# Optimization experiments

Measured on AMD Instinct MI355X. Metric: run time of the kernel, lower is better.

The kernel has to match this reference:

```python
import jax, jax.numpy as jnp
import numpy as np

HEAD_SIZE = 64

def setup_inputs() -> dict:
    key = jax.random.key(0)
    k1, k2, k3, k4 = jax.random.split(key, 4)
    B, T, C = 4, 4096, 768
    s = 1.0 / np.sqrt(C)
    return {
        "x": jax.random.normal(k1, (B, T, C), dtype=jnp.float32),
        "Wq": jax.random.normal(k2, (C, HEAD_SIZE), dtype=jnp.float32) * s,
        "Wk": jax.random.normal(k3, (C, HEAD_SIZE), dtype=jnp.float32) * s,
        "Wv": jax.random.normal(k4, (C, HEAD_SIZE), dtype=jnp.float32) * s,
    }

def reference(x, Wq, Wk, Wv):
    # x: [B,T,C]; Wq/Wk/Wv: [C,H]
    T = x.shape[1]
    q = jnp.einsum('btc,ch->bth', x, Wq)
    k = jnp.einsum('btc,ch->bth', x, Wk)
    v = jnp.einsum('btc,ch->bth', x, Wv)
    scale = HEAD_SIZE ** (-0.5)
    wei = jnp.einsum('bth,bsh->bts', q, k) * scale  # [B,T,T]
    causal = jnp.tril(jnp.ones((T, T), dtype=bool))
    wei = jnp.where(causal, wei, -jnp.inf)
    wei = jax.nn.softmax(wei, axis=-1)
    # dropout p=0.0 -> identity
    out = jnp.einsum('bts,bsh->bth', wei, v)  # [B,T,H]
    return out
```

## Files before the change

### kernel.cpp

```cpp
#include <hip/hip_runtime.h>
#include <hip/hip_bf16.h>
#include <stdint.h>

typedef unsigned short u16;
typedef __attribute__((ext_vector_type(8))) __bf16 bf16x8;
typedef __attribute__((ext_vector_type(4))) float f32x4;

#define LOG2E 1.44269504088896340736f

__device__ inline u16 f2bf(float f){
  uint32_t u = __float_as_uint(f);
  u += 0x7FFFu + ((u >> 16) & 1u);
  return (u16)(u >> 16);
}
__device__ inline float bf2f(u16 v){
  return __uint_as_float(((uint32_t)v) << 16);
}

typedef const __attribute__((address_space(1))) void* gas_t;
typedef __attribute__((address_space(3))) void* las_t;
__device__ inline void gl_lds16(const void* g, void* l){
  __builtin_amdgcn_global_load_lds((gas_t)g, (las_t)l, 16, 0, 0);
}

__global__ __launch_bounds__(256) void wt_kernel(const float* __restrict__ Wq,
                                                 const float* __restrict__ Wk,
                                                 const float* __restrict__ Wv,
                                                 u16* __restrict__ wtf){
  int idx = blockIdx.x * 256 + threadIdx.x;
  if (idx >= 192 * 768) return;
  int n = idx / 768, c = idx - n * 768;
  int h = n & 63;
  const float* W = (n < 64) ? Wq : ((n < 128) ? Wk : Wv);
  float v = W[c * 64 + h];
  if (n < 64) v *= 0.125f * LOG2E;
  int f = n >> 4, n16 = n & 15;
  int kstep = c >> 5, quad = (c >> 3) & 3, j = c & 7;
  wtf[(size_t)((f * 24 + kstep) * 64 + quad * 16 + n16) * 8 + j] = f2bf(v);
}

__global__ __launch_bounds__(256) void proj_kernel(const float* __restrict__ x,
                                                   const u16* __restrict__ wtf,
                                                   u16* __restrict__ qs,
                                                   u16* __restrict__ ksf,
                                                   u16* __restrict__ vtf){
  __shared__ u16 At[24 * 64 * 8];
  const int tid = threadIdx.x;
  const int w = tid >> 6, lane = tid & 63;
  const int n16 = lane & 15, quad = lane >> 4;
  const int rt = blockIdx.x * 16;

  const float* xb = x + (size_t)rt * 768;
  float4 t[12];
#pragma unroll
  for (int i = 0; i < 12; ++i)
    t[i] = *(const float4*)(xb + (size_t)(i * 256 + tid) * 4);
#pragma unroll
  for (int i = 0; i < 12; ++i){
    int l = i * 256 + tid;
    int row = l / 192, c4 = l - row * 192;
    int ksn = c4 >> 3, qd = (c4 >> 1) & 3, j0 = (c4 & 1) * 4;
    int idx = ((ksn * 64 + qd * 16 + row) * 8 + j0) ^ ((ksn & 7) << 3);
    union { ushort4 s; u16 e[4]; } pk;
    pk.e[0] = f2bf(t[i].x); pk.e[1] = f2bf(t[i].y);
    pk.e[2] = f2bf(t[i].z); pk.e[3] = f2bf(t[i].w);
    *(ushort4*)&At[idx] = pk.s;
  }
  __syncthreads();

  const f32x4 fz = {0.f, 0.f, 0.f, 0.f};
  f32x4 acc[3];
#pragma unroll
  for (int j = 0; j < 3; ++j) acc[j] = fz;

#pragma unroll
  for (int kst = 0; kst < 24; ++kst){
    const int sw = (kst & 7) << 3;
    bf16x8 a = *(const bf16x8*)&At[((kst * 64 + lane) * 8) ^ sw];
#pragma unroll
    for (int j = 0; j < 3; ++j){
      bf16x8 bfr = *(const bf16x8*)(wtf + (size_t)(((3 * w + j) * 24 + kst) * 64 + lane) * 8);
      acc[j] = __builtin_amdgcn_mfma_f32_16x16x32_bf16(a, bfr, acc[j], 0, 0, 0);
    }
  }
  __syncthreads();

#pragma unroll
  for (int j = 0; j < 3; ++j){
    const int F = 3 * w + j;
    const int s = F >> 2, c0 = (F & 3) * 16;
#pragma unroll
    for (int r = 0; r < 4; ++r){
      u16 val = f2bf(acc[j][r]);
      int row = quad * 4 + r;
      if (s < 2) At[s * 1152 + row * 72 + c0 + n16] = val;
      else       At[2304 + (c0 + n16) * 24 + row]   = val;
    }
  }
  __syncthreads();

  const int bb = rt >> 12, t0 = rt & 4095;
  const int kt = t0 >> 6;
  const int fk = (t0 >> 4) & 3;
  const int half0 = (t0 >> 5) & 1;
  const int qhalf = (t0 >> 4) & 1;
  if (tid < 128){
    int row = tid >> 3, hc = tid & 7;
    uint4 qv = *(const uint4*)&At[row * 72 + hc * 8];
    *(uint4*)(qs + (size_t)(rt + row) * 64 + hc * 8) = qv;
  } else {
    int tt = tid - 128;
    int half = tt >> 6, l2 = tt & 63;
    int nn = l2 & 15, qq = l2 >> 4;
    uint4 kv = *(const uint4*)&At[1152 + nn * 72 + half * 32 + qq * 8];
    size_t off = ((((size_t)(bb * 64 + kt) * 4 + fk) * 2 + half) * 64 + l2) * 8;
    *(uint4*)(ksf + off) = kv;
  }
  if (tid < 128){
    int f = tid >> 5, idx5 = tid & 31;
    int qsel = idx5 >> 4, nn = idx5 & 15;
    int h = f * 16 + nn;
    uint4 vv = *(const uint4*)&At[2304 + h * 24 + qsel * 8];
    int lane2 = (2 * qhalf + qsel) * 16 + nn;
    size_t off = ((((size_t)(bb * 64 + kt) * 4 + f) * 2 + half0) * 64 + lane2) * 8;
    *(uint4*)(vtf + off) = vv;
  }
}

__global__ __launch_bounds__(256) void flash_part(const u16* __restrict__ qs,
                                                  const u16* __restrict__ ksf,
                                                  const u16* __restrict__ vtf,
                                                  u16* __restrict__ Opart,
                                                  float* __restrict__ ml){
  const int b  = blockIdx.x >> 9;
  const int qt = (blockIdx.x >> 4) & 31;
  const int ck = blockIdx.x & 15;
  const int kt0 = ck * 4;
  const int ktmax = 2 * qt + 1;
  if (kt0 > ktmax) return;
  const int nt = min(ktmax, kt0 + 3) - kt0 + 1;

  __shared__ u16 Kb[2][4096];
  __shared__ u16 Vb[2][4096];
  __shared__ u16 Ps[128 * 72];
  const int tid = threadIdx.x;
  const int w = tid >> 6, lane = tid & 63;
  const int n16 = lane & 15, quad = lane >> 4;

  const u16* qb  = qs  + (size_t)b * 262144;
  const u16* kpg = ksf + (size_t)b * 262144 + (size_t)kt0 * 4096;
  const u16* vpg = vtf + (size_t)b * 262144 + (size_t)kt0 * 4096;

  bf16x8 qA[2][2];
#pragma unroll
  for (int m = 0; m < 2; ++m){
    const size_t qrow = (size_t)(qt * 128 + w * 32 + m * 16 + n16) * 64;
    qA[m][0] = *(const bf16x8*)(qb + qrow + quad * 8);
    qA[m][1] = *(const bf16x8*)(qb + qrow + 32 + quad * 8);
  }

  const f32x4 fz = {0.f, 0.f, 0.f, 0.f};
  f32x4 O[2][4];
  float rs[2][4];
#pragma unroll
  for (int m = 0; m < 2; ++m)
#pragma unroll
    for (int f = 0; f < 4; ++f){ O[m][f] = fz; rs[m][f] = 0.f; }

#define STAGE(bf, ti)                                                        \
  {                                                                          \
    const u16* kg = kpg + (size_t)(ti) * 4096 + (w * 2) * 512 + lane * 8;    \
    const u16* vg = vpg + (size_t)(ti) * 4096 + (w * 2) * 512 + lane * 8;    \
    gl_lds16(kg,       &Kb[bf][(w * 2 + 0) * 512]);                          \
    gl_lds16(kg + 512, &Kb[bf][(w * 2 + 1) * 512]);                          \
    gl_lds16(vg,       &Vb[bf][(w * 2 + 0) * 512]);                          \
    gl_lds16(vg + 512, &Vb[bf][(w * 2 + 1) * 512]);                          \
  }

  STAGE(0, 0);
  __syncthreads();
  int c = 0;

  for (int it = 0; it < nt; ++it){
    const int kt = kt0 + it;
    if (it + 1 < nt) STAGE(c ^ 1, it + 1);

    f32x4 S[2][4];
#pragma unroll
    for (int f = 0; f < 4; ++f){
      bf16x8 k0 = *(const bf16x8*)&Kb[c][(f * 2 + 0) * 512 + lane * 8];
      bf16x8 k1 = *(const bf16x8*)&Kb[c][(f * 2 + 1) * 512 + lane * 8];
#pragma unroll
      for (int m = 0; m < 2; ++m){
        f32x4 s = fz;
        s = __builtin_amdgcn_mfma_f32_16x16x32_bf16(qA[m][0], k0, s, 0, 0, 0);
        s = __builtin_amdgcn_mfma_f32_16x16x32_bf16(qA[m][1], k1, s, 0, 0, 0);
        S[m][f] = s;
      }
    }

    if (kt >= 2 * qt){
#pragma unroll
      for (int m = 0; m < 2; ++m)
#pragma unroll
        for (int f = 0; f < 4; ++f)
#pragma unroll
          for (int r = 0; r < 4; ++r){
            int col = kt * 64 + f * 16 + n16;
            int row = qt * 128 + w * 32 + m * 16 + quad * 4 + r;
            if (col > row) S[m][f][r] = -1e30f;
          }
    }

#pragma unroll
    for (int m = 0; m < 2; ++m)
#pragma unroll
      for (int f = 0; f < 4; ++f)
#pragma unroll
        for (int r = 0; r < 4; ++r){
          float p = __builtin_amdgcn_exp2f(S[m][f][r]);
          S[m][f][r] = p;
          rs[m][r] += p;
        }

#pragma unroll
    for (int m = 0; m < 2; ++m)
#pragma unroll
      for (int f = 0; f < 4; ++f){
        u16* p = &Ps[(w * 32 + m * 16 + quad * 4) * 72 + f * 16 + n16];
        p[0]   = f2bf(S[m][f][0]);
        p[72]  = f2bf(S[m][f][1]);
        p[144] = f2bf(S[m][f][2]);
        p[216] = f2bf(S[m][f][3]);
      }
    bf16x8 pA[2][2];
#pragma unroll
    for (int m = 0; m < 2; ++m){
      pA[m][0] = *(const bf16x8*)&Ps[(w * 32 + m * 16 + n16) * 72 + quad * 8];
      pA[m][1] = *(const bf16x8*)&Ps[(w * 32 + m * 16 + n16) * 72 + 32 + quad * 8];
    }

#pragma unroll
    for (int f = 0; f < 4; ++f){
      bf16x8 v0 = *(const bf16x8*)&Vb[c][(f * 2 + 0) * 512 + lane * 8];
      bf16x8 v1 = *(const bf16x8*)&Vb[c][(f * 2 + 1) * 512 + lane * 8];
#pragma unroll
      for (int m = 0; m < 2; ++m){
        O[m][f] = __builtin_amdgcn_mfma_f32_16x16x32_bf16(pA[m][0], v0, O[m][f], 0, 0, 0);
        O[m][f] = __builtin_amdgcn_mfma_f32_16x16x32_bf16(pA[m][1], v1, O[m][f], 0, 0, 0);
      }
    }

    __syncthreads();
    c ^= 1;
  }
#undef STAGE

#pragma unroll
  for (int m = 0; m < 2; ++m)
#pragma unroll
    for (int r = 0; r < 4; ++r){
#pragma unroll
      for (int off = 1; off < 16; off <<= 1)
        rs[m][r] += __shfl_xor(rs[m][r], off, 16);
    }

  const size_t oidx = (size_t)blockIdx.x * 8192;
#pragma unroll
  for (int m = 0; m < 2; ++m)
#pragma unroll
    for (int f = 0; f < 4; ++f)
#pragma unroll
      for (int r = 0; r < 4; ++r){
        int row_local = w * 32 + m * 16 + quad * 4 + r;
        Opart[oidx + (size_t)row_local * 64 + f * 16 + n16] = f2bf(O[m][f][r]);
      }
  if (n16 == 0){
    float* lp = ml + (size_t)blockIdx.x * 128;
#pragma unroll
    for (int m = 0; m < 2; ++m)
#pragma unroll
      for (int r = 0; r < 4; ++r)
        lp[w * 32 + m * 16 + quad * 4 + r] = rs[m][r];
  }
}

__global__ __launch_bounds__(256) void combine_kernel(const u16* __restrict__ Opart,
                                                      const float* __restrict__ ml,
                                                      float* __restrict__ out){
  const int gid = blockIdx.x * 256 + threadIdx.x;
  const int bq = gid >> 11;
  const int rem = (gid & 2047) * 4;
  const int row = rem >> 6;
  const int qt = bq & 31;
  const int nc = (2 * qt + 5) >> 2;

  float L = 0.f;
  float a0 = 0.f, a1 = 0.f, a2 = 0.f, a3 = 0.f;
  for (int c = 0; c < nc; ++c){
    L += ml[((size_t)bq * 16 + c) * 128 + row];
    const u16* p = Opart + ((size_t)bq * 16 + c) * 8192 + rem;
    uint2 d = *(const uint2*)p;
    a0 += bf2f((u16)(d.x & 0xffffu));
    a1 += bf2f((u16)(d.x >> 16));
    a2 += bf2f((u16)(d.y & 0xffffu));
    a3 += bf2f((u16)(d.y >> 16));
  }
  const float invL = 1.0f / L;
  float4 v = {a0 * invL, a1 * invL, a2 * invL, a3 * invL};
  *(float4*)(out + (size_t)gid * 4) = v;
}

extern "C" void kernel_launch(void* const* d_in, const int* in_sizes, int n_in,
                              void* d_out, int out_size, void* d_ws, size_t ws_size,
                              hipStream_t stream){
  const float* x  = (const float*)d_in[0];
  const float* Wq = (const float*)d_in[1];
  const float* Wk = (const float*)d_in[2];
  const float* Wv = (const float*)d_in[3];
  float* out = (float*)d_out;

  u16* qs  = (u16*)d_ws;
  u16* ksf = qs  + (size_t)16384 * 64;
  u16* vtf = ksf + (size_t)16384 * 64;
  u16* wtf = vtf + (size_t)16384 * 64;
  u16* Opart = wtf + (size_t)192 * 768;
  float* ml = (float*)(Opart + (size_t)2048 * 8192);

  wt_kernel<<<576, 256, 0, stream>>>(Wq, Wk, Wv, wtf);
  proj_kernel<<<1024, 256, 0, stream>>>(x, wtf, qs, ksf, vtf);
  flash_part<<<2048, 256, 0, stream>>>(qs, ksf, vtf, Opart, ml);
  combine_kernel<<<1024, 256, 0, stream>>>(Opart, ml, out);
}
```

Before: 139.9 us.

## Compact causal work grid and single-buffer K/V staging in flash kernel

Replaces the 2048-block grid, where many blocks exit early on the causal mask, with a dense 1088-block grid. The new grid maps block ids to (qt, chunk) pairs through an integer square-root decode: full 4-tile chunks come first and 2-tile diagonal chunks after. The combine kernel is updated to the new partial-result indexing. K/V staging drops from double buffering to a single buffer with sync before and after each load, which halves that LDS use and may raise occupancy, but the next tile's load no longer overlaps compute.

```diff
diff --git a/kernel.cpp b/kernel.cpp
--- a/kernel.cpp
+++ b/kernel.cpp
@@ -1,6 +1,7 @@
 #include <hip/hip_runtime.h>
 #include <hip/hip_bf16.h>
 #include <stdint.h>
+#include <math.h>
 
 typedef unsigned short u16;
 typedef __attribute__((ext_vector_type(8))) __bf16 bf16x8;
@@ -132,16 +133,28 @@
                                                   const u16* __restrict__ vtf,
                                                   u16* __restrict__ Opart,
                                                   float* __restrict__ ml){
-  const int b  = blockIdx.x >> 9;
-  const int qt = (blockIdx.x >> 4) & 31;
-  const int ck = blockIdx.x & 15;
+  const int gid = blockIdx.x;
+  int b, qt, ck, nt;
+  if (gid < 1024){
+    b = gid >> 8;
+    int r = gid & 255;
+    int m = (int)sqrtf((float)r);
+    if (m * m > r) --m;
+    if ((m + 1) * (m + 1) <= r) ++m;
+    int d = r - m * m;
+    if (d < m){ qt = 2 * m;     ck = d;     }
+    else      { qt = 2 * m + 1; ck = d - m; }
+    nt = 4;
+  } else {
+    int t = gid - 1024;
+    b = t >> 4;
+    int m = t & 15;
+    qt = 2 * m; ck = m; nt = 2;
+  }
   const int kt0 = ck * 4;
-  const int ktmax = 2 * qt + 1;
-  if (kt0 > ktmax) return;
-  const int nt = min(ktmax, kt0 + 3) - kt0 + 1;
-
-  __shared__ u16 Kb[2][4096];
-  __shared__ u16 Vb[2][4096];
+
+  __shared__ u16 Kb[4096];
+  __shared__ u16 Vb[4096];
   __shared__ u16 Ps[128 * 72];
   const int tid = threadIdx.x;
   const int w = tid >> 6, lane = tid & 63;
@@ -167,29 +180,27 @@
 #pragma unroll
     for (int f = 0; f < 4; ++f){ O[m][f] = fz; rs[m][f] = 0.f; }
 
-#define STAGE(bf, ti)                                                        \
+#define STAGE(ti)                                                            \
   {                                                                          \
     const u16* kg = kpg + (size_t)(ti) * 4096 + (w * 2) * 512 + lane * 8;    \
     const u16* vg = vpg + (size_t)(ti) * 4096 + (w * 2) * 512 + lane * 8;    \
-    gl_lds16(kg,       &Kb[bf][(w * 2 + 0) * 512]);                          \
-    gl_lds16(kg + 512, &Kb[bf][(w * 2 + 1) * 512]);                          \
-    gl_lds16(vg,       &Vb[bf][(w * 2 + 0) * 512]);                          \
-    gl_lds16(vg + 512, &Vb[bf][(w * 2 + 1) * 512]);                          \
-  }
-
-  STAGE(0, 0);
-  __syncthreads();
-  int c = 0;
+    gl_lds16(kg,       &Kb[(w * 2 + 0) * 512]);                              \
+    gl_lds16(kg + 512, &Kb[(w * 2 + 1) * 512]);                              \
+    gl_lds16(vg,       &Vb[(w * 2 + 0) * 512]);                              \
+    gl_lds16(vg + 512, &Vb[(w * 2 + 1) * 512]);                              \
+  }
 
   for (int it = 0; it < nt; ++it){
     const int kt = kt0 + it;
-    if (it + 1 < nt) STAGE(c ^ 1, it + 1);
+    if (it) __syncthreads();
+    STAGE(it);
+    __syncthreads();
 
     f32x4 S[2][4];
 #pragma unroll
     for (int f = 0; f < 4; ++f){
-      bf16x8 k0 = *(const bf16x8*)&Kb[c][(f * 2 + 0) * 512 + lane * 8];
-      bf16x8 k1 = *(const bf16x8*)&Kb[c][(f * 2 + 1) * 512 + lane * 8];
+      bf16x8 k0 = *(const bf16x8*)&Kb[(f * 2 + 0) * 512 + lane * 8];
+      bf16x8 k1 = *(const bf16x8*)&Kb[(f * 2 + 1) * 512 + lane * 8];
 #pragma unroll
       for (int m = 0; m < 2; ++m){
         f32x4 s = fz;
@@ -242,17 +253,14 @@
 
 #pragma unroll
     for (int f = 0; f < 4; ++f){
-      bf16x8 v0 = *(const bf16x8*)&Vb[c][(f * 2 + 0) * 512 + lane * 8];
-      bf16x8 v1 = *(const bf16x8*)&Vb[c][(f * 2 + 1) * 512 + lane * 8];
+      bf16x8 v0 = *(const bf16x8*)&Vb[(f * 2 + 0) * 512 + lane * 8];
+      bf16x8 v1 = *(const bf16x8*)&Vb[(f * 2 + 1) * 512 + lane * 8];
 #pragma unroll
       for (int m = 0; m < 2; ++m){
         O[m][f] = __builtin_amdgcn_mfma_f32_16x16x32_bf16(pA[m][0], v0, O[m][f], 0, 0, 0);
         O[m][f] = __builtin_amdgcn_mfma_f32_16x16x32_bf16(pA[m][1], v1, O[m][f], 0, 0, 0);
       }
     }
-
-    __syncthreads();
-    c ^= 1;
   }
 #undef STAGE
 
@@ -265,7 +273,7 @@
         rs[m][r] += __shfl_xor(rs[m][r], off, 16);
     }
 
-  const size_t oidx = (size_t)blockIdx.x * 8192;
+  const size_t oidx = (size_t)gid * 8192;
 #pragma unroll
   for (int m = 0; m < 2; ++m)
 #pragma unroll
@@ -276,7 +284,7 @@
         Opart[oidx + (size_t)row_local * 64 + f * 16 + n16] = f2bf(O[m][f][r]);
       }
   if (n16 == 0){
-    float* lp = ml + (size_t)blockIdx.x * 128;
+    float* lp = ml + (size_t)gid * 128;
 #pragma unroll
     for (int m = 0; m < 2; ++m)
 #pragma unroll
@@ -292,15 +300,28 @@
   const int bq = gid >> 11;
   const int rem = (gid & 2047) * 4;
   const int row = rem >> 6;
-  const int qt = bq & 31;
-  const int nc = (2 * qt + 5) >> 2;
+  const int b = bq >> 5, qt = bq & 31;
+  const int m = qt >> 1;
+  const int nc4 = (qt & 1) ? (m + 1) : m;
+  const int F = (qt & 1) ? (m * m + m) : (m * m);
 
   float L = 0.f;
   float a0 = 0.f, a1 = 0.f, a2 = 0.f, a3 = 0.f;
-  for (int c = 0; c < nc; ++c){
-    L += ml[((size_t)bq * 16 + c) * 128 + row];
-    const u16* p = Opart + ((size_t)bq * 16 + c) * 8192 + rem;
-    uint2 d = *(const uint2*)p;
+  for (int j = 0; j < nc4; ++j){
+    int p = b * 256 + F + j;
+    L += ml[(size_t)p * 128 + row];
+    const u16* q = Opart + (size_t)p * 8192 + rem;
+    uint2 d = *(const uint2*)q;
+    a0 += bf2f((u16)(d.x & 0xffffu));
+    a1 += bf2f((u16)(d.x >> 16));
+    a2 += bf2f((u16)(d.y & 0xffffu));
+    a3 += bf2f((u16)(d.y >> 16));
+  }
+  if (!(qt & 1)){
+    int p = 1024 + b * 16 + m;
+    L += ml[(size_t)p * 128 + row];
+    const u16* q = Opart + (size_t)p * 8192 + rem;
+    uint2 d = *(const uint2*)q;
     a0 += bf2f((u16)(d.x & 0xffffu));
     a1 += bf2f((u16)(d.x >> 16));
     a2 += bf2f((u16)(d.y & 0xffffu));
@@ -325,10 +346,10 @@
   u16* vtf = ksf + (size_t)16384 * 64;
   u16* wtf = vtf + (size_t)16384 * 64;
   u16* Opart = wtf + (size_t)192 * 768;
-  float* ml = (float*)(Opart + (size_t)2048 * 8192);
+  float* ml = (float*)(Opart + (size_t)1088 * 8192);
 
   wt_kernel<<<576, 256, 0, stream>>>(Wq, Wk, Wv, wtf);
   proj_kernel<<<1024, 256, 0, stream>>>(x, wtf, qs, ksf, vtf);
-  flash_part<<<2048, 256, 0, stream>>>(qs, ksf, vtf, Opart, ml);
+  flash_part<<<1088, 256, 0, stream>>>(qs, ksf, vtf, Opart, ml);
   combine_kernel<<<1024, 256, 0, stream>>>(Opart, ml, out);
 }
```

New measurement: 131.1 us. -6.3%, faster.
